# Kernel optimization log

Hardware: AMD Instinct MI355X
Metric: run time of the kernel (lower is better)

The kernel has to match this reference:

```python
import jax, jax.numpy as jnp
import numpy as np
from jax import lax

SZ, SENLEN, V, DWE, DPE, MAXPOS, DEE, DR, DC, KLOC = 2048, 128, 50000, 100, 5, 256, 100, 34, 300, 10
CIN = DWE + 2 * DPE + DEE  # 210


def setup_inputs() -> dict:
    key = jax.random.key(0)
    ks = jax.random.split(key, 16)
    inp = jax.random.randint(ks[0], (SZ, SENLEN), 0, V, dtype=jnp.int32)
    pos1 = jax.random.randint(ks[1], (SZ, SENLEN), 0, MAXPOS, dtype=jnp.int32)
    pos2 = jax.random.randint(ks[2], (SZ, SENLEN), 0, MAXPOS, dtype=jnp.int32)
    loc = jax.random.randint(ks[3], (SZ, KLOC), 0, V, dtype=jnp.int32)
    loc_mark = jax.random.randint(ks[4], (SZ,), 1, 6, dtype=jnp.int32)  # 1..5, keeps 4+mark < KLOC
    subtype = jax.random.randint(ks[5], (SZ,), 0, DR, dtype=jnp.int32)
    # piecewise L/M/R sentence masks around two cut points
    a = jax.random.randint(ks[6], (SZ, 1), 1, SENLEN // 2, dtype=jnp.int32)
    b = jax.random.randint(ks[7], (SZ, 1), SENLEN // 2, SENLEN - 1, dtype=jnp.int32)
    ar = jnp.arange(SENLEN)[None, :]
    maskL = (ar < a).astype(jnp.float32)
    maskM = ((ar >= a) & (ar < b)).astype(jnp.float32)
    maskR = (ar >= b).astype(jnp.float32)
    word_emb = 0.1 * jax.random.normal(ks[8], (V, DWE), dtype=jnp.float32)
    pos_emb = 0.1 * jax.random.normal(ks[9], (MAXPOS, DPE), dtype=jnp.float32)
    event_emb = 0.1 * jax.random.normal(ks[10], (DR, DEE), dtype=jnp.float32)
    conv_w = (1.0 / np.sqrt(CIN * 3)) * jax.random.normal(ks[11], (DC, CIN, 3), dtype=jnp.float32)
    conv_b = 0.01 * jax.random.normal(ks[12], (DC,), dtype=jnp.float32)
    return dict(inp=inp, pos1=pos1, pos2=pos2, loc=loc, loc_mark=loc_mark, subtype=subtype,
                maskL=maskL, maskM=maskM, maskR=maskR, word_emb=word_emb, pos_emb=pos_emb,
                event_emb=event_emb, conv_w=conv_w, conv_b=conv_b)


def reference(inp, pos1, pos2, loc, loc_mark, subtype, maskL, maskM, maskR,
              word_emb, pos_emb, event_emb, conv_w, conv_b):
    # padding_idx=0 semantics
    W = word_emb.at[0].set(0.0)
    E = event_emb.at[0].set(0.0)

    embeds = W[inp]                       # (SZ, L, DWE)
    p1 = pos_emb[pos1]                    # (SZ, L, DPE)
    p2 = pos_emb[pos2]                    # (SZ, L, DPE)

    # ragged loc feature: l[4] <- mean(l[4:4+mark]); l[5] <- l[4+mark]; keep l[0:6]
    loc_e = W[loc]                        # (SZ, K, DWE)
    j = jnp.arange(KLOC)[None, :]
    sel = ((j >= 4) & (j < 4 + loc_mark[:, None])).astype(loc_e.dtype)  # (SZ, K)
    mean4 = jnp.einsum('skd,sk->sd', loc_e, sel) / loc_mark[:, None].astype(loc_e.dtype)
    new5 = jnp.take_along_axis(loc_e, (4 + loc_mark)[:, None, None], axis=1)[:, 0, :]
    loc_embeds = jnp.concatenate([loc_e[:, :4].reshape(loc_e.shape[0], -1), mean4, new5], axis=1)  # (SZ, 6*DWE)

    ev = jnp.broadcast_to(E[subtype][:, None, :], (subtype.shape[0], SENLEN, DEE))
    x = jnp.concatenate([embeds, p1, p2, ev], axis=2).transpose(0, 2, 1)  # (SZ, CIN, L)

    conved = lax.conv_general_dilated(x, conv_w, window_strides=(1,), padding=((1, 1),),
                                      dimension_numbers=('NCH', 'OIH', 'NCH'))
    conved = conved + conv_b[None, :, None]  # (SZ, DC, L)

    # (mask*x + 1) -> maxpool over L -> -1  ==  max over L of mask*x (the +/-1 cancels exactly)
    pooledL = jnp.max(conved * maskL[:, None, :], axis=2)
    pooledM = jnp.max(conved * maskM[:, None, :], axis=2)
    pooledR = jnp.max(conved * maskR[:, None, :], axis=2)
    pooled = jnp.concatenate([pooledL, pooledM, pooledR], axis=1)  # (SZ, 3*DC)

    rep = jnp.tanh(jnp.concatenate([pooled, loc_embeds], axis=1))  # dropout in eval = identity
    return rep
```

## Files before the change

kernel.cpp:

```cpp
#include <hip/hip_runtime.h>
#include <hip/hip_bf16.h>

#define SZ    2048
#define SLEN  128
#define DWE   100
#define DPE   5
#define DEE   100
#define DC    300
#define CIN   210
#define KLOC  10
#define OUTW  1500
#define DR    34

#define KP    128
#define LCOLS 136
#define LROWS 130
#define CPAD  320

typedef short short8 __attribute__((ext_vector_type(8)));
typedef float f32x4 __attribute__((ext_vector_type(4)));

static __device__ __forceinline__ unsigned short f2b(float f) {
  return __builtin_bit_cast(unsigned short, __float2bfloat16(f));
}

__global__ void prep_wk(const float* __restrict__ conv_w, unsigned short* __restrict__ wk) {
  int idx = blockIdx.x * 256 + threadIdx.x;
  if (idx >= 3 * CPAD * KP) return;
  int i  = idx & (KP - 1);
  int c  = (idx / KP) % CPAD;
  int kk = idx / (KP * CPAD);
  float v = 0.f;
  if (c < DC && i < 110) v = conv_w[(c * CIN + i) * 3 + kk];
  wk[idx] = f2b(v);
}

__global__ void prep_ev(const float* __restrict__ conv_w, const float* __restrict__ event_emb,
                        const float* __restrict__ conv_b, float* __restrict__ evconv) {
  int idx = blockIdx.x * 256 + threadIdx.x;
  if (idx >= DR * 3 * DC) return;
  int c  = idx % DC;
  int kk = (idx / DC) % 3;
  int st = idx / (3 * DC);
  float v = 0.f;
  if (st != 0) {
    const float* wrow = conv_w + (c * CIN + 110) * 3 + kk;
    const float* e = event_emb + st * DEE;
    for (int i = 0; i < DEE; ++i) v += wrow[3 * i] * e[i];
  }
  if (kk == 1) v += conv_b[c];
  evconv[idx] = v;
}

__global__ __launch_bounds__(512, 4) void dmcnn_main(
    const int* __restrict__ inp, const int* __restrict__ pos1, const int* __restrict__ pos2,
    const int* __restrict__ loc, const int* __restrict__ loc_mark, const int* __restrict__ subtype,
    const float* __restrict__ maskL, const float* __restrict__ maskM, const float* __restrict__ maskR,
    const float* __restrict__ word_emb, const float* __restrict__ pos_emb,
    const unsigned short* __restrict__ wk, const float* __restrict__ evconv,
    float* __restrict__ out)
{
  __shared__ unsigned short XT[LROWS * LCOLS];
  __shared__ float pool[2 * CPAD * 4];
  __shared__ int cw[4];

  const int s   = blockIdx.x;
  const int tid = threadIdx.x;

  if (tid < 64)        ((unsigned*)XT)[tid] = 0u;
  else if (tid < 128)  ((unsigned*)(XT + 129 * LCOLS))[tid - 64] = 0u;

  if (tid < 128) {
    const int inL = maskL[s * SLEN + tid] > 0.5f;
    const int inM = maskM[s * SLEN + tid] > 0.5f;
    unsigned long long bL = __ballot(inL);
    unsigned long long bM = __ballot(inM);
    if ((tid & 63) == 0) {
      cw[tid >> 6]       = __popcll(bL);
      cw[2 + (tid >> 6)] = __popcll(bM);
    }
  }

  {
    const int t = tid >> 2, q = tid & 3;
    unsigned short* row = &XT[(t + 1) * LCOLS];
    if (q < 2) {
      const int w = inp[s * SLEN + t];
      const float* wp = word_emb + (size_t)w * DWE + q * 50;
      #pragma unroll
      for (int j = 0; j < 25; ++j) {
        unsigned u = 0u;
        if (w != 0) {
          float2 v = ((const float2*)wp)[j];
          u = (unsigned)f2b(v.x) | ((unsigned)f2b(v.y) << 16);
        }
        *(unsigned*)&row[q * 50 + j * 2] = u;
      }
    } else {
      const int p = (q == 2 ? pos1 : pos2)[s * SLEN + t];
      const float* pp = pos_emb + p * DPE;
      #pragma unroll
      for (int d = 0; d < DPE; ++d) row[DWE + (q - 2) * DPE + d] = f2b(pp[d]);
      #pragma unroll
      for (int d = 0; d < 9; ++d) row[110 + 9 * (q - 2) + d] = 0;
    }
  }
  __syncthreads();

  const int wv   = tid >> 6;
  const int wc   = wv & 3, wt = wv >> 2;
  const int lane = tid & 63;
  const int r16  = lane & 15, q16 = lane >> 4;

  f32x4 acc[4][5];
  #pragma unroll
  for (int tt = 0; tt < 4; ++tt)
    #pragma unroll
    for (int ci = 0; ci < 5; ++ci) acc[tt][ci] = (f32x4){0.f, 0.f, 0.f, 0.f};

  const unsigned short* wbase = wk + (size_t)(80 * wc + r16) * KP + q16 * 8;
  #pragma unroll 1
  for (int ks = 0; ks < 12; ++ks) {
    const int kk = ks >> 2, kt = ks & 3;
    short8 wf[5];
    #pragma unroll
    for (int ci = 0; ci < 5; ++ci)
      wf[ci] = *(const short8*)(wbase + (size_t)(kk * CPAD + 16 * ci) * KP + kt * 32);
    #pragma unroll
    for (int tt = 0; tt < 4; ++tt) {
      short8 xf = *(const short8*)&XT[(64 * wt + 16 * tt + r16 + kk) * LCOLS + kt * 32 + q16 * 8];
      #pragma unroll
      for (int ci = 0; ci < 5; ++ci)
        acc[tt][ci] = __builtin_amdgcn_mfma_f32_16x16x32_bf16(xf, wf[ci], acc[tt][ci], 0, 0, 0);
    }
  }

  const int acut = cw[0] + cw[1];
  const int bcut = acut + cw[2] + cw[3];
  const int st   = subtype[s];
  const float* evc = evconv + (size_t)st * 3 * DC;
  float* orow = out + (size_t)s * OUTW;

  #pragma unroll
  for (int ci = 0; ci < 5; ++ci) {
    const int c = 80 * wc + 16 * ci + r16;
    const int cc = c < DC ? c : 0;
    const float s0 = evc[cc], s1 = evc[cc + DC], s2 = evc[cc + 2 * DC];
    const float base = s0 + s1 + s2;
    float rL = 0.f, rM = 0.f, rR = 0.f;
    #pragma unroll
    for (int tt = 0; tt < 4; ++tt) {
      #pragma unroll
      for (int j = 0; j < 4; ++j) {
        const int t = 64 * wt + 16 * tt + 4 * q16 + j;
        float v = acc[tt][ci][j] + base;
        if (t == 0)   v -= s0;
        if (t == 127) v -= s2;
        if (t < acut)      rL = fmaxf(rL, v);
        else if (t < bcut) rM = fmaxf(rM, v);
        else               rR = fmaxf(rR, v);
      }
    }
    #pragma unroll
    for (int off = 16; off < 64; off <<= 1) {
      rL = fmaxf(rL, __shfl_xor(rL, off));
      rM = fmaxf(rM, __shfl_xor(rM, off));
      rR = fmaxf(rR, __shfl_xor(rR, off));
    }
    if (q16 == 0) {
      float* p = pool + ((size_t)wt * CPAD + c) * 4;
      p[0] = rL; p[1] = rM; p[2] = rR;
    }
  }

  __syncthreads();
  if (tid < DC) {
    const float* p0 = pool + (size_t)tid * 4;
    const float* p1 = pool + (size_t)(CPAD + tid) * 4;
    orow[tid]          = tanhf(fmaxf(p0[0], p1[0]));
    orow[DC + tid]     = tanhf(fmaxf(p0[1], p1[1]));
    orow[2 * DC + tid] = tanhf(fmaxf(p0[2], p1[2]));
  }

  const int mark = loc_mark[s];
  for (int j = tid; j < 600; j += 512) {
    float v;
    if (j < 400) {
      const int k = j / 100, d = j % 100;
      const int idx = loc[s * KLOC + k];
      v = (idx == 0) ? 0.f : word_emb[(size_t)idx * DWE + d];
    } else if (j < 500) {
      const int d = j - 400;
      float sum = 0.f;
      for (int k = 4; k < 4 + mark; ++k) {
        const int idx = loc[s * KLOC + k];
        sum += (idx == 0) ? 0.f : word_emb[(size_t)idx * DWE + d];
      }
      v = sum / (float)mark;
    } else {
      const int d = j - 500;
      const int idx = loc[s * KLOC + 4 + mark];
      v = (idx == 0) ? 0.f : word_emb[(size_t)idx * DWE + d];
    }
    orow[900 + j] = tanhf(v);
  }
}

extern "C" void kernel_launch(void* const* d_in, const int* in_sizes, int n_in,
                              void* d_out, int out_size, void* d_ws, size_t ws_size,
                              hipStream_t stream) {
  const int*   inp       = (const int*)d_in[0];
  const int*   pos1      = (const int*)d_in[1];
  const int*   pos2      = (const int*)d_in[2];
  const int*   loc       = (const int*)d_in[3];
  const int*   loc_mark  = (const int*)d_in[4];
  const int*   subtype   = (const int*)d_in[5];
  const float* maskL     = (const float*)d_in[6];
  const float* maskM     = (const float*)d_in[7];
  const float* maskR     = (const float*)d_in[8];
  const float* word_emb  = (const float*)d_in[9];
  const float* pos_emb   = (const float*)d_in[10];
  const float* event_emb = (const float*)d_in[11];
  const float* conv_w    = (const float*)d_in[12];
  const float* conv_b    = (const float*)d_in[13];

  unsigned short* wk = (unsigned short*)d_ws;
  float* evconv = (float*)((char*)d_ws + 3 * CPAD * KP * 2);
  float* out = (float*)d_out;

  prep_wk<<<(3 * CPAD * KP + 255) / 256, 256, 0, stream>>>(conv_w, wk);
  prep_ev<<<(DR * 3 * DC + 255) / 256, 256, 0, stream>>>(conv_w, event_emb, conv_b, evconv);
  dmcnn_main<<<SZ, 512, 0, stream>>>(inp, pos1, pos2, loc, loc_mark, subtype,
      maskL, maskM, maskR, word_emb, pos_emb, wk, evconv, out);
}
```

Before: 268.9 us.

## Vectorize embedding gather, split prep_ev reduction across lanes, use fast tanh

The word-embedding gather now has all four threads per token load float4 chunks and convert them with packed bf16 conversion instead of two threads doing float2 loads. prep_ev splits each 100-term dot product across four lanes and combines them with shuffles, giving more parallelism in that setup kernel. tanhf is replaced by an exp/rcp approximation with clamping, which may change results slightly.

```diff
diff --git a/kernel.cpp b/kernel.cpp
--- a/kernel.cpp
+++ b/kernel.cpp
@@ -24,6 +24,18 @@
   return __builtin_bit_cast(unsigned short, __float2bfloat16(f));
 }
 
+static __device__ __forceinline__ unsigned cvt_pk_bf16(float lo, float hi) {
+  unsigned r;
+  asm volatile("v_cvt_pk_bf16_f32 %0, %1, %2" : "=v"(r) : "v"(lo), "v"(hi));
+  return r;
+}
+
+static __device__ __forceinline__ float ftanh(float x) {
+  x = fminf(fmaxf(x, -15.f), 15.f);
+  float e = __expf(2.0f * x);
+  return (e - 1.0f) * __builtin_amdgcn_rcpf(e + 1.0f);
+}
+
 __global__ void prep_wk(const float* __restrict__ conv_w, unsigned short* __restrict__ wk) {
   int idx = blockIdx.x * 256 + threadIdx.x;
   if (idx >= 3 * CPAD * KP) return;
@@ -37,19 +49,22 @@
 
 __global__ void prep_ev(const float* __restrict__ conv_w, const float* __restrict__ event_emb,
                         const float* __restrict__ conv_b, float* __restrict__ evconv) {
-  int idx = blockIdx.x * 256 + threadIdx.x;
-  if (idx >= DR * 3 * DC) return;
-  int c  = idx % DC;
-  int kk = (idx / DC) % 3;
-  int st = idx / (3 * DC);
+  int gid = blockIdx.x * 256 + threadIdx.x;
+  int o = gid >> 2, sub = gid & 3;
+  if (o >= DR * 3 * DC) return;
+  int c  = o % DC;
+  int kk = (o / DC) % 3;
+  int st = o / (3 * DC);
   float v = 0.f;
   if (st != 0) {
     const float* wrow = conv_w + (c * CIN + 110) * 3 + kk;
     const float* e = event_emb + st * DEE;
-    for (int i = 0; i < DEE; ++i) v += wrow[3 * i] * e[i];
-  }
-  if (kk == 1) v += conv_b[c];
-  evconv[idx] = v;
+    #pragma unroll
+    for (int i = 0; i < 25; ++i) v += wrow[3 * (sub * 25 + i)] * e[sub * 25 + i];
+  }
+  v += __shfl_xor(v, 1);
+  v += __shfl_xor(v, 2);
+  if (sub == 0) evconv[o] = v + (kk == 1 ? conv_b[c] : 0.f);
 }
 
 __global__ __launch_bounds__(512, 4) void dmcnn_main(
@@ -84,25 +99,23 @@
   {
     const int t = tid >> 2, q = tid & 3;
     unsigned short* row = &XT[(t + 1) * LCOLS];
-    if (q < 2) {
-      const int w = inp[s * SLEN + t];
-      const float* wp = word_emb + (size_t)w * DWE + q * 50;
-      #pragma unroll
-      for (int j = 0; j < 25; ++j) {
-        unsigned u = 0u;
-        if (w != 0) {
-          float2 v = ((const float2*)wp)[j];
-          u = (unsigned)f2b(v.x) | ((unsigned)f2b(v.y) << 16);
-        }
-        *(unsigned*)&row[q * 50 + j * 2] = u;
-      }
-    } else {
-      const int p = (q == 2 ? pos1 : pos2)[s * SLEN + t];
+    const int w = inp[s * SLEN + t];
+    const float4* wp = (const float4*)(word_emb + (size_t)w * DWE);
+    for (int j = q; j < 25; j += 4) {
+      float4 v = wp[j];
+      unsigned lo = cvt_pk_bf16(v.x, v.y);
+      unsigned hi = cvt_pk_bf16(v.z, v.w);
+      if (w == 0) { lo = 0u; hi = 0u; }
+      *(uint2*)&row[4 * j] = make_uint2(lo, hi);
+    }
+    if (q == 1 || q == 2) {
+      const int p = (q == 1 ? pos1 : pos2)[s * SLEN + t];
       const float* pp = pos_emb + p * DPE;
       #pragma unroll
-      for (int d = 0; d < DPE; ++d) row[DWE + (q - 2) * DPE + d] = f2b(pp[d]);
-      #pragma unroll
-      for (int d = 0; d < 9; ++d) row[110 + 9 * (q - 2) + d] = 0;
+      for (int d = 0; d < DPE; ++d) row[DWE + (q - 1) * DPE + d] = f2b(pp[d]);
+    } else if (q == 3) {
+      #pragma unroll
+      for (int d = 0; d < 9; ++d) *(unsigned*)&row[110 + 2 * d] = 0u;
     }
   }
   __syncthreads();
@@ -177,9 +190,9 @@
   if (tid < DC) {
     const float* p0 = pool + (size_t)tid * 4;
     const float* p1 = pool + (size_t)(CPAD + tid) * 4;
-    orow[tid]          = tanhf(fmaxf(p0[0], p1[0]));
-    orow[DC + tid]     = tanhf(fmaxf(p0[1], p1[1]));
-    orow[2 * DC + tid] = tanhf(fmaxf(p0[2], p1[2]));
+    orow[tid]          = ftanh(fmaxf(p0[0], p1[0]));
+    orow[DC + tid]     = ftanh(fmaxf(p0[1], p1[1]));
+    orow[2 * DC + tid] = ftanh(fmaxf(p0[2], p1[2]));
   }
 
   const int mark = loc_mark[s];
@@ -202,7 +215,7 @@
       const int idx = loc[s * KLOC + 4 + mark];
       v = (idx == 0) ? 0.f : word_emb[(size_t)idx * DWE + d];
     }
-    orow[900 + j] = tanhf(v);
+    orow[900 + j] = ftanh(v);
   }
 }
 
@@ -229,7 +242,7 @@
   float* out = (float*)d_out;
 
   prep_wk<<<(3 * CPAD * KP + 255) / 256, 256, 0, stream>>>(conv_w, wk);
-  prep_ev<<<(DR * 3 * DC + 255) / 256, 256, 0, stream>>>(conv_w, event_emb, conv_b, evconv);
+  prep_ev<<<(DR * 3 * DC * 4 + 255) / 256, 256, 0, stream>>>(conv_w, event_emb, conv_b, evconv);
   dmcnn_main<<<SZ, 512, 0, stream>>>(inp, pos1, pos2, loc, loc_mark, subtype,
       maskL, maskM, maskR, word_emb, pos_emb, wk, evconv, out);
 }
```

After: 248.2 us. -7.7%, faster.
